# Kernel optimization log

Measured on AMD Instinct MI355X. Metric: run time of the kernel, lower is better.

The kernel has to match this reference:

```python
import jax, jax.numpy as jnp
import numpy as np

BS, SEQ, DK = 4, 4096, 128

def setup_inputs() -> dict:
    key = jax.random.key(0)
    kq, kk, kv = jax.random.split(key, 3)
    q = jax.random.normal(kq, (BS, SEQ, DK), dtype=jnp.float32)
    k = jax.random.normal(kk, (BS, SEQ, DK), dtype=jnp.float32)
    v = jax.random.normal(kv, (BS, SEQ, DK), dtype=jnp.float32)
    return {"q": q, "k": k, "v": v}

def reference(q, k, v):
    d_k = q.shape[-1]
    # scores: [bs, s_q, s_k]
    scaled = jnp.einsum('bqd,bkd->bqk', q, k) / jnp.sqrt(jnp.asarray(d_k, q.dtype))
    # NOTE: original torch code applies softmax over dim=1 (query axis), faithfully reproduced here.
    attn = jax.nn.softmax(scaled, axis=1)
    return jnp.einsum('bqk,bkd->bqd', attn, v)
```

## Files before the change

kernel.cpp:

```cpp
#include <hip/hip_runtime.h>
#include <hip/hip_bf16.h>

#define BS  4
#define SEQ 4096
#define DK  128

#define C1_SCALE (1.4426950408889634f / 11.313708498984761f)

typedef __attribute__((ext_vector_type(8))) short bf16x8;
typedef __attribute__((ext_vector_type(4))) float f32x4;
typedef unsigned short ushort_t;

__device__ inline unsigned pk_bf16(float a, float b) {
    __hip_bfloat162 h = __float22bfloat162_rn(make_float2(a, b));
    union { __hip_bfloat162 h2; unsigned u; } cv;
    cv.h2 = h;
    return cv.u;
}

__device__ inline bf16x8 pk8(float4 a, float4 b) {
    union { bf16x8 v; unsigned u[4]; } r;
    r.u[0] = pk_bf16(a.x, a.y);
    r.u[1] = pk_bf16(a.z, a.w);
    r.u[2] = pk_bf16(b.x, b.y);
    r.u[3] = pk_bf16(b.z, b.w);
    return r.v;
}

__device__ inline void gld_lds16(const ushort_t* g, ushort_t* l) {
    __builtin_amdgcn_global_load_lds(
        (const __attribute__((address_space(1))) unsigned int*)g,
        (__attribute__((address_space(3))) unsigned int*)l,
        16, 0, 0);
}

__device__ inline void bar_fence() {
    __builtin_amdgcn_s_barrier();
    asm volatile("" ::: "memory");
}

__global__ __launch_bounds__(256) void cast_qk_sw(
    const float* __restrict__ Q, const float* __restrict__ K,
    ushort_t* __restrict__ Qb, ushort_t* __restrict__ Kb)
{
    const int g = blockIdx.x * 256 + threadIdx.x;
    const int q = g >> 4, ap = g & 15;
    const int a = ap ^ (q & 15);
    const float* src = Q + (size_t)q * DK + a * 8;
    float4 x = *(const float4*)src, y = *(const float4*)(src + 4);
    x.x *= C1_SCALE; x.y *= C1_SCALE; x.z *= C1_SCALE; x.w *= C1_SCALE;
    y.x *= C1_SCALE; y.y *= C1_SCALE; y.z *= C1_SCALE; y.w *= C1_SCALE;
    *(bf16x8*)(Qb + (size_t)g * 8) = pk8(x, y);
    src = K + (size_t)q * DK + a * 8;
    float4 x2 = *(const float4*)src, y2 = *(const float4*)(src + 4);
    *(bf16x8*)(Kb + (size_t)g * 8) = pk8(x2, y2);
}

__global__ __launch_bounds__(256) void sdpa_lsum(
    const ushort_t* __restrict__ Qb, const ushort_t* __restrict__ Kb,
    float* __restrict__ lp)
{
    __shared__ ushort_t Qs[3][4096];

    const int kt = blockIdx.x, qs = blockIdx.y, b = blockIdx.z;
    const int tid = threadIdx.x;
    const int w = tid >> 6, lane = tid & 63, ln = lane & 15, quad = lane >> 4;

    bf16x8 ka[2][4];
#pragma unroll
    for (int mt = 0; mt < 2; ++mt)
#pragma unroll
        for (int c = 0; c < 4; ++c)
            ka[mt][c] = *(const bf16x8*)(Kb +
                ((size_t)(b * SEQ) + kt * 128 + w * 32 + mt * 16 + ln) * DK +
                (((c * 4 + quad) ^ ln) * 8));

    float ls[2][4] = {};
    const ushort_t* qtb = Qb + ((size_t)(b * SEQ + qs * 512)) * DK;

#define A_DMA(BUF, I)                                                          \
    {                                                                          \
        _Pragma("unroll")                                                      \
        for (int j = 0; j < 2; ++j)                                            \
            gld_lds16(qtb + (size_t)(I) * 4096 + (j * 256 + tid) * 8,          \
                      &Qs[BUF][(j * 256 + w * 64) * 8]);                       \
    }

#define A_CMP(BUF)                                                             \
    {                                                                          \
        bf16x8 qf[2][4];                                                       \
        _Pragma("unroll")                                                      \
        for (int nt = 0; nt < 2; ++nt)                                         \
            _Pragma("unroll")                                                  \
            for (int c = 0; c < 4; ++c)                                        \
                qf[nt][c] = *(const bf16x8*)&Qs[BUF][(nt * 16 + ln) * 128 +    \
                                    (((c * 4 + quad) ^ ln) * 8)];              \
        _Pragma("unroll")                                                      \
        for (int mt = 0; mt < 2; ++mt)                                         \
            _Pragma("unroll")                                                  \
            for (int nt = 0; nt < 2; ++nt) {                                   \
                f32x4 s = {0.f, 0.f, 0.f, 0.f};                                \
                __builtin_amdgcn_s_setprio(1);                                 \
                _Pragma("unroll")                                              \
                for (int c = 0; c < 4; ++c)                                    \
                    s = __builtin_amdgcn_mfma_f32_16x16x32_bf16(               \
                        ka[mt][c], qf[nt][c], s, 0, 0, 0);                     \
                __builtin_amdgcn_s_setprio(0);                                 \
                _Pragma("unroll")                                              \
                for (int r = 0; r < 4; ++r)                                    \
                    ls[mt][r] += __builtin_amdgcn_exp2f(s[r]);                 \
            }                                                                  \
    }

    A_DMA(0, 0)
    A_DMA(1, 1)
    for (int t = 0; t < 15; ++t) {
        asm volatile("s_waitcnt vmcnt(2) lgkmcnt(0)" ::: "memory");
        bar_fence();
        if (t < 14) A_DMA((t + 2) % 3, t + 2)
        A_CMP(t % 3)
    }
    asm volatile("s_waitcnt vmcnt(0) lgkmcnt(0)" ::: "memory");
    bar_fence();
    A_CMP(0)
#undef A_DMA
#undef A_CMP

#pragma unroll
    for (int mt = 0; mt < 2; ++mt)
#pragma unroll
        for (int r = 0; r < 4; ++r) {
            float vv = ls[mt][r];
            vv += __shfl_xor(vv, 1);
            vv += __shfl_xor(vv, 2);
            vv += __shfl_xor(vv, 4);
            vv += __shfl_xor(vv, 8);
            ls[mt][r] = vv;
        }
    if (ln < 8) {
        int k = kt * 128 + w * 32 + (ln >> 2) * 16 + quad * 4 + (ln & 3);
        lp[((size_t)(qs * BS + b)) * SEQ + k] = ls[ln >> 2][ln & 3];
    }
}

__global__ __launch_bounds__(256) void vb_transpose(
    const float* __restrict__ V, const float* __restrict__ lp,
    ushort_t* __restrict__ VbT)
{
    __shared__ float Vl[64][132];
    __shared__ float Wl[64];

    const int kt = blockIdx.x, b = blockIdx.y;
    const int tid = threadIdx.x;
    const int k0 = kt * 64;
    {
        int r = tid >> 2, sg = tid & 3;
        const float* src = V + ((size_t)(b * SEQ) + k0 + r) * DK + sg * 32;
#pragma unroll
        for (int i = 0; i < 8; ++i)
            *(float4*)&Vl[r][sg * 32 + i * 4] = *(const float4*)(src + i * 4);
    }
    if (tid < 64) {
        float s = 0.f;
#pragma unroll
        for (int qs = 0; qs < 8; ++qs)
            s += lp[((size_t)(qs * BS + b)) * SEQ + k0 + tid];
        Wl[tid] = 1.0f / s;
    }
    __syncthreads();

    const int d = tid >> 1, kh = tid & 1;
    unsigned u[16];
#pragma unroll
    for (int j = 0; j < 16; ++j) {
        int row = kh * 32 + j * 2;
        u[j] = pk_bf16(Vl[row][d] * Wl[row], Vl[row + 1][d] * Wl[row + 1]);
    }
    ushort_t* dst = VbT + ((size_t)(b * DK) + d) * SEQ + k0 + kh * 32;
#pragma unroll
    for (int i = 0; i < 4; ++i) {
        uint4 t4; t4.x = u[i*4]; t4.y = u[i*4+1]; t4.z = u[i*4+2]; t4.w = u[i*4+3];
        *(uint4*)(dst + i * 8) = t4;
    }
}

__global__ __launch_bounds__(256) void sdpa_out(
    const ushort_t* __restrict__ Qb, const ushort_t* __restrict__ Kb,
    const ushort_t* __restrict__ VbT,
    float* __restrict__ Op, float* __restrict__ O, int use_partial)
{
    __shared__ ushort_t Kt[2][8192];
    __shared__ ushort_t Vt[2][8192];
    __shared__ ushort_t Pt[4096];

    const int g  = blockIdx.x;
    const int qt = blockIdx.y;
    const int ks = g >> 2, b = g & 3;
    const int tid = threadIdx.x;
    const int w = tid >> 6, lane = tid & 63, ln = lane & 15, quad = lane >> 4;

    bf16x8 qa[4][4];
#pragma unroll
    for (int nt = 0; nt < 4; ++nt)
#pragma unroll
        for (int c = 0; c < 4; ++c)
            qa[c][nt] = *(const bf16x8*)(Qb +
                ((size_t)(b * SEQ) + qt * 64 + nt * 16 + ln) * DK +
                (((c * 4 + quad) ^ ln) * 8));

    f32x4 acc[4][2];
#pragma unroll
    for (int i = 0; i < 4; ++i)
#pragma unroll
        for (int j = 0; j < 2; ++j) acc[i][j] = (f32x4){0.f, 0.f, 0.f, 0.f};

    const ushort_t* ksrc = Kb + ((size_t)(b * SEQ) + ks * 1024) * DK;
    const ushort_t* vsrc = VbT + ((size_t)(b * DK)) * SEQ + ks * 1024;
    const int vd = tid >> 3, vap = tid & 7;

#define O_DMA(BUF, PH)                                                         \
    {                                                                          \
        _Pragma("unroll")                                                      \
        for (int j = 0; j < 4; ++j)                                            \
            gld_lds16(ksrc + (size_t)(PH) * 64 * DK + (j * 256 + tid) * 8,     \
                      &Kt[BUF][(j * 256 + w * 64) * 8]);                       \
        _Pragma("unroll")                                                      \
        for (int j = 0; j < 4; ++j)                                            \
            gld_lds16(vsrc + (size_t)(j * 32 + vd) * SEQ + (PH) * 64 +         \
                          ((vap ^ (vd & 7)) * 8),                              \
                      &Vt[BUF][(j * 256 + w * 64) * 8]);                       \
    }

#define QK_PHASE(BUF)                                                          \
    {                                                                          \
        bf16x8 kf[4];                                                          \
        _Pragma("unroll")                                                      \
        for (int c = 0; c < 4; ++c)                                            \
            kf[c] = *(const bf16x8*)&Kt[BUF][(w * 16 + ln) * 128 +             \
                                             (((c * 4 + quad) ^ ln) * 8)];     \
        _Pragma("unroll")                                                      \
        for (int nt = 0; nt < 4; ++nt) {                                       \
            f32x4 s = {0.f, 0.f, 0.f, 0.f};                                    \
            __builtin_amdgcn_s_setprio(1);                                     \
            _Pragma("unroll")                                                  \
            for (int c = 0; c < 4; ++c)                                        \
                s = __builtin_amdgcn_mfma_f32_16x16x32_bf16(kf[c], qa[c][nt], s, 0, 0, 0); \
            __builtin_amdgcn_s_setprio(0);                                     \
            uint2 pw;                                                          \
            pw.x = pk_bf16(__builtin_amdgcn_exp2f(s[0]),                       \
                           __builtin_amdgcn_exp2f(s[1]));                      \
            pw.y = pk_bf16(__builtin_amdgcn_exp2f(s[2]),                       \
                           __builtin_amdgcn_exp2f(s[3]));                      \
            const int q = nt * 16 + ln;                                        \
            const int a16 = w * 2 + (quad >> 1);                               \
            *(uint2*)&Pt[q * 64 + ((a16 ^ (q & 7)) * 8) + (quad & 1) * 4] = pw; \
        }                                                                      \
    }

#define PV_PHASE(BUF)                                                          \
    {                                                                          \
        _Pragma("unroll")                                                      \
        for (int kc = 0; kc < 2; ++kc) {                                       \
            bf16x8 pa[4], vfr[2];                                              \
            _Pragma("unroll")                                                  \
            for (int qf2 = 0; qf2 < 4; ++qf2)                                  \
                pa[qf2] = *(const bf16x8*)&Pt[(qf2 * 16 + ln) * 64 +           \
                                    (((kc * 4 + quad) ^ (ln & 7)) * 8)];       \
            _Pragma("unroll")                                                  \
            for (int dt = 0; dt < 2; ++dt)                                     \
                vfr[dt] = *(const bf16x8*)&Vt[BUF][(w * 32 + dt * 16 + ln) * 64 + \
                                    (((kc * 4 + quad) ^ (ln & 7)) * 8)];       \
            __builtin_amdgcn_s_setprio(1);                                     \
            _Pragma("unroll")                                                  \
            for (int qf2 = 0; qf2 < 4; ++qf2)                                  \
                _Pragma("unroll")                                              \
                for (int dt = 0; dt < 2; ++dt)                                 \
                    acc[qf2][dt] = __builtin_amdgcn_mfma_f32_16x16x32_bf16(    \
                        pa[qf2], vfr[dt], acc[qf2][dt], 0, 0, 0);              \
            __builtin_amdgcn_s_setprio(0);                                     \
        }                                                                      \
    }

    O_DMA(0, 0)
    O_DMA(1, 1)
    for (int ph = 0; ph < 15; ++ph) {
        const int cur = ph & 1;
        asm volatile("s_waitcnt vmcnt(8)" ::: "memory");
        bar_fence();
        QK_PHASE(cur)
        asm volatile("s_waitcnt lgkmcnt(0)" ::: "memory");
        bar_fence();
        PV_PHASE(cur)
        asm volatile("s_waitcnt lgkmcnt(0)" ::: "memory");
        bar_fence();
        if (ph < 14) O_DMA(cur, ph + 2)
    }
    asm volatile("s_waitcnt vmcnt(0)" ::: "memory");
    bar_fence();
    QK_PHASE(1)
    asm volatile("s_waitcnt lgkmcnt(0)" ::: "memory");
    bar_fence();
    PV_PHASE(1)
#undef O_DMA
#undef QK_PHASE
#undef PV_PHASE

    if (use_partial) {
        float* dst = Op + (size_t)ks * ((size_t)BS * SEQ * DK) +
                     ((size_t)(b * SEQ) + qt * 64 + quad * 4) * DK + w * 32 + ln;
#pragma unroll
        for (int qf2 = 0; qf2 < 4; ++qf2)
#pragma unroll
            for (int dt = 0; dt < 2; ++dt)
#pragma unroll
                for (int r = 0; r < 4; ++r)
                    dst[((size_t)(qf2 * 16 + r)) * DK + dt * 16] = acc[qf2][dt][r];
    } else {
#pragma unroll
        for (int qf2 = 0; qf2 < 4; ++qf2)
#pragma unroll
            for (int dt = 0; dt < 2; ++dt)
#pragma unroll
                for (int r = 0; r < 4; ++r)
                    atomicAdd(&O[((size_t)(b * SEQ) + qt * 64 + qf2 * 16 + quad * 4 + r) * DK +
                                 w * 32 + dt * 16 + ln], acc[qf2][dt][r]);
    }
}

__global__ __launch_bounds__(256) void reduce4(
    const float* __restrict__ Op, float* __restrict__ O)
{
    const size_t N = (size_t)BS * SEQ * DK;
    size_t i = ((size_t)blockIdx.x * 256 + threadIdx.x) * 4;
    float4 a0 = *(const float4*)(Op + i);
    float4 a1 = *(const float4*)(Op + N + i);
    float4 a2 = *(const float4*)(Op + 2 * N + i);
    float4 a3 = *(const float4*)(Op + 3 * N + i);
    float4 r;
    r.x = a0.x + a1.x + a2.x + a3.x;
    r.y = a0.y + a1.y + a2.y + a3.y;
    r.z = a0.z + a1.z + a2.z + a3.z;
    r.w = a0.w + a1.w + a2.w + a3.w;
    *(float4*)(O + i) = r;
}

extern "C" void kernel_launch(void* const* d_in, const int* in_sizes, int n_in,
                              void* d_out, int out_size, void* d_ws, size_t ws_size,
                              hipStream_t stream) {
    const float* q = (const float*)d_in[0];
    const float* k = (const float*)d_in[1];
    const float* v = (const float*)d_in[2];
    float* out = (float*)d_out;

    const size_t QKV = (size_t)BS * SEQ * DK;
    float*    lp  = (float*)d_ws;
    ushort_t* Qb  = (ushort_t*)((char*)d_ws + (1 << 20));
    ushort_t* Kb  = Qb + QKV;
    ushort_t* VbT = Kb + QKV;
    float*    Op  = (float*)(VbT + QKV);

    const size_t need_p = (1u << 20) + 3 * QKV * 2 + 4 * QKV * sizeof(float);

    cast_qk_sw<<<dim3(BS * SEQ * 16 / 256), 256, 0, stream>>>(q, k, Qb, Kb);
    sdpa_lsum  <<<dim3(32, 8, 4), 256, 0, stream>>>(Qb, Kb, lp);
    vb_transpose<<<dim3(64, 4),   256, 0, stream>>>(v, lp, VbT);

    if (ws_size >= need_p) {
        sdpa_out<<<dim3(16, 64), 256, 0, stream>>>(Qb, Kb, VbT, Op, out, 1);
        reduce4 <<<dim3(BS * SEQ * DK / 4 / 256), 256, 0, stream>>>(Op, out);
    } else {
        hipMemsetAsync(out, 0, QKV * sizeof(float), stream);
        sdpa_out<<<dim3(16, 64), 256, 0, stream>>>(Qb, Kb, VbT, nullptr, out, 0);
    }
}
```

Baseline: 153.1 us.

## Software-pipeline QK and PV phases in sdpa_out and halve key splits

Restructures the sdpa_out main loop so the QK scores and exponentials for the next tile are computed while PV runs on the current tile. P is double-buffered in LDS and the exp results are held in registers across iterations, which cuts the barriers per tile from three to one. Key splitting drops from 4 to 2 chunks of 2048 keys, halving the partial-output buffer and reduce traffic but also halving the grid to 512 blocks. Launch bounds now request 2 blocks per CU, which adds register pressure and LDS use in exchange for overlap.

```diff
diff --git a/kernel.cpp b/kernel.cpp
--- a/kernel.cpp
+++ b/kernel.cpp
@@ -184,20 +184,21 @@
     }
 }
 
-__global__ __launch_bounds__(256) void sdpa_out(
+__global__ __launch_bounds__(256, 2) void sdpa_out(
     const ushort_t* __restrict__ Qb, const ushort_t* __restrict__ Kb,
     const ushort_t* __restrict__ VbT,
     float* __restrict__ Op, float* __restrict__ O, int use_partial)
 {
     __shared__ ushort_t Kt[2][8192];
     __shared__ ushort_t Vt[2][8192];
-    __shared__ ushort_t Pt[4096];
+    __shared__ ushort_t Pt[2][4096];
 
     const int g  = blockIdx.x;
     const int qt = blockIdx.y;
     const int ks = g >> 2, b = g & 3;
     const int tid = threadIdx.x;
     const int w = tid >> 6, lane = tid & 63, ln = lane & 15, quad = lane >> 4;
+    const int vd2 = lane >> 3, va2 = lane & 7;
 
     bf16x8 qa[4][4];
 #pragma unroll
@@ -214,24 +215,27 @@
 #pragma unroll
         for (int j = 0; j < 2; ++j) acc[i][j] = (f32x4){0.f, 0.f, 0.f, 0.f};
 
-    const ushort_t* ksrc = Kb + ((size_t)(b * SEQ) + ks * 1024) * DK;
-    const ushort_t* vsrc = VbT + ((size_t)(b * DK)) * SEQ + ks * 1024;
-    const int vd = tid >> 3, vap = tid & 7;
-
-#define O_DMA(BUF, PH)                                                         \
+    const ushort_t* ksrc = Kb + ((size_t)(b * SEQ) + ks * 2048) * DK;
+    const ushort_t* vsrc = VbT + ((size_t)(b * DK)) * SEQ + ks * 2048;
+
+#define DMA_K(BUF, T)                                                          \
     {                                                                          \
         _Pragma("unroll")                                                      \
         for (int j = 0; j < 4; ++j)                                            \
-            gld_lds16(ksrc + (size_t)(PH) * 64 * DK + (j * 256 + tid) * 8,     \
-                      &Kt[BUF][(j * 256 + w * 64) * 8]);                       \
+            gld_lds16(ksrc + ((size_t)(T) * 64 + w * 16 + j * 4 + quad) * DK + \
+                          ln * 8,                                              \
+                      &Kt[BUF][(w * 256 + j * 64) * 8]);                       \
+    }
+#define DMA_V(BUF, T)                                                          \
+    {                                                                          \
         _Pragma("unroll")                                                      \
         for (int j = 0; j < 4; ++j)                                            \
-            gld_lds16(vsrc + (size_t)(j * 32 + vd) * SEQ + (PH) * 64 +         \
-                          ((vap ^ (vd & 7)) * 8),                              \
-                      &Vt[BUF][(j * 256 + w * 64) * 8]);                       \
-    }
-
-#define QK_PHASE(BUF)                                                          \
+            gld_lds16(vsrc + (size_t)(w * 32 + j * 8 + vd2) * SEQ +            \
+                          (T) * 64 + ((va2 ^ vd2) * 8),                        \
+                      &Vt[BUF][(w * 256 + j * 64) * 8]);                       \
+    }
+
+#define QK_COMPUTE(BUF, PW)                                                    \
     {                                                                          \
         bf16x8 kf[4];                                                          \
         _Pragma("unroll")                                                      \
@@ -246,14 +250,20 @@
             for (int c = 0; c < 4; ++c)                                        \
                 s = __builtin_amdgcn_mfma_f32_16x16x32_bf16(kf[c], qa[c][nt], s, 0, 0, 0); \
             __builtin_amdgcn_s_setprio(0);                                     \
-            uint2 pw;                                                          \
-            pw.x = pk_bf16(__builtin_amdgcn_exp2f(s[0]),                       \
-                           __builtin_amdgcn_exp2f(s[1]));                      \
-            pw.y = pk_bf16(__builtin_amdgcn_exp2f(s[2]),                       \
-                           __builtin_amdgcn_exp2f(s[3]));                      \
+            PW[nt].x = pk_bf16(__builtin_amdgcn_exp2f(s[0]),                   \
+                               __builtin_amdgcn_exp2f(s[1]));                  \
+            PW[nt].y = pk_bf16(__builtin_amdgcn_exp2f(s[2]),                   \
+                               __builtin_amdgcn_exp2f(s[3]));                  \
+        }                                                                      \
+    }
+
+#define PT_WRITE(PW, P)                                                        \
+    {                                                                          \
+        _Pragma("unroll")                                                      \
+        for (int nt = 0; nt < 4; ++nt) {                                       \
             const int q = nt * 16 + ln;                                        \
             const int a16 = w * 2 + (quad >> 1);                               \
-            *(uint2*)&Pt[q * 64 + ((a16 ^ (q & 7)) * 8) + (quad & 1) * 4] = pw; \
+            *(uint2*)&Pt[P][q * 64 + ((a16 ^ (q & 7)) * 8) + (quad & 1) * 4] = PW[nt]; \
         }                                                                      \
     }
 
@@ -264,7 +274,7 @@
             bf16x8 pa[4], vfr[2];                                              \
             _Pragma("unroll")                                                  \
             for (int qf2 = 0; qf2 < 4; ++qf2)                                  \
-                pa[qf2] = *(const bf16x8*)&Pt[(qf2 * 16 + ln) * 64 +           \
+                pa[qf2] = *(const bf16x8*)&Pt[BUF][(qf2 * 16 + ln) * 64 +      \
                                     (((kc * 4 + quad) ^ (ln & 7)) * 8)];       \
             _Pragma("unroll")                                                  \
             for (int dt = 0; dt < 2; ++dt)                                     \
@@ -281,28 +291,46 @@
         }                                                                      \
     }
 
-    O_DMA(0, 0)
-    O_DMA(1, 1)
-    for (int ph = 0; ph < 15; ++ph) {
-        const int cur = ph & 1;
-        asm volatile("s_waitcnt vmcnt(8)" ::: "memory");
-        bar_fence();
-        QK_PHASE(cur)
-        asm volatile("s_waitcnt lgkmcnt(0)" ::: "memory");
-        bar_fence();
-        PV_PHASE(cur)
-        asm volatile("s_waitcnt lgkmcnt(0)" ::: "memory");
-        bar_fence();
-        if (ph < 14) O_DMA(cur, ph + 2)
-    }
-    asm volatile("s_waitcnt vmcnt(0)" ::: "memory");
+#define O_ITER(T, CUR, PWRD, PWWR)                                             \
+    {                                                                          \
+        PT_WRITE(PWRD, CUR)                                                    \
+        DMA_K(CUR, (T) + 2)                                                    \
+        asm volatile("s_waitcnt vmcnt(8) lgkmcnt(0)" ::: "memory");            \
+        bar_fence();                                                           \
+        QK_COMPUTE((CUR) ^ 1, PWWR)                                            \
+        PV_PHASE(CUR)                                                          \
+        asm volatile("s_waitcnt lgkmcnt(0)" ::: "memory");                     \
+        DMA_V(CUR, (T) + 2)                                                    \
+    }
+
+    uint2 pwA[4], pwB[4];
+
+    DMA_K(0, 0)
+    DMA_V(0, 0)
+    DMA_K(1, 1)
+    DMA_V(1, 1)
+    asm volatile("s_waitcnt vmcnt(12)" ::: "memory");
+    QK_COMPUTE(0, pwA)
+
+    for (int tt = 0; tt < 15; ++tt) {
+        const int t0 = 2 * tt;
+        O_ITER(t0,     0, pwA, pwB)
+        O_ITER(t0 + 1, 1, pwB, pwA)
+    }
+    PT_WRITE(pwA, 0)
+    asm volatile("s_waitcnt vmcnt(4) lgkmcnt(0)" ::: "memory");
     bar_fence();
-    QK_PHASE(1)
-    asm volatile("s_waitcnt lgkmcnt(0)" ::: "memory");
+    QK_COMPUTE(1, pwB)
+    PV_PHASE(0)
+    PT_WRITE(pwB, 1)
+    asm volatile("s_waitcnt vmcnt(0) lgkmcnt(0)" ::: "memory");
     bar_fence();
     PV_PHASE(1)
-#undef O_DMA
-#undef QK_PHASE
+#undef O_ITER
+#undef DMA_K
+#undef DMA_V
+#undef QK_COMPUTE
+#undef PT_WRITE
 #undef PV_PHASE
 
     if (use_partial) {
@@ -327,20 +355,18 @@
     }
 }
 
-__global__ __launch_bounds__(256) void reduce4(
+__global__ __launch_bounds__(256) void reduce2(
     const float* __restrict__ Op, float* __restrict__ O)
 {
     const size_t N = (size_t)BS * SEQ * DK;
     size_t i = ((size_t)blockIdx.x * 256 + threadIdx.x) * 4;
     float4 a0 = *(const float4*)(Op + i);
     float4 a1 = *(const float4*)(Op + N + i);
-    float4 a2 = *(const float4*)(Op + 2 * N + i);
-    float4 a3 = *(const float4*)(Op + 3 * N + i);
     float4 r;
-    r.x = a0.x + a1.x + a2.x + a3.x;
-    r.y = a0.y + a1.y + a2.y + a3.y;
-    r.z = a0.z + a1.z + a2.z + a3.z;
-    r.w = a0.w + a1.w + a2.w + a3.w;
+    r.x = a0.x + a1.x;
+    r.y = a0.y + a1.y;
+    r.z = a0.z + a1.z;
+    r.w = a0.w + a1.w;
     *(float4*)(O + i) = r;
 }
 
@@ -359,17 +385,17 @@
     ushort_t* VbT = Kb + QKV;
     float*    Op  = (float*)(VbT + QKV);
 
-    const size_t need_p = (1u << 20) + 3 * QKV * 2 + 4 * QKV * sizeof(float);
+    const size_t need_p = (1u << 20) + 3 * QKV * 2 + 2 * QKV * sizeof(float);
 
     cast_qk_sw<<<dim3(BS * SEQ * 16 / 256), 256, 0, stream>>>(q, k, Qb, Kb);
     sdpa_lsum  <<<dim3(32, 8, 4), 256, 0, stream>>>(Qb, Kb, lp);
     vb_transpose<<<dim3(64, 4),   256, 0, stream>>>(v, lp, VbT);
 
     if (ws_size >= need_p) {
-        sdpa_out<<<dim3(16, 64), 256, 0, stream>>>(Qb, Kb, VbT, Op, out, 1);
-        reduce4 <<<dim3(BS * SEQ * DK / 4 / 256), 256, 0, stream>>>(Op, out);
+        sdpa_out<<<dim3(8, 64), 256, 0, stream>>>(Qb, Kb, VbT, Op, out, 1);
+        reduce2<<<dim3(BS * SEQ * DK / 4 / 256), 256, 0, stream>>>(Op, out);
     } else {
         hipMemsetAsync(out, 0, QKV * sizeof(float), stream);
-        sdpa_out<<<dim3(16, 64), 256, 0, stream>>>(Qb, Kb, VbT, nullptr, out, 0);
-    }
-}
+        sdpa_out<<<dim3(8, 64), 256, 0, stream>>>(Qb, Kb, VbT, nullptr, out, 0);
+    }
+}
```

Result: faster. 147.7 us (-3.5%).

## Rewrite sdpa_out with 32x32 MFMA, register-resident P and 128-query tiles

Applied to the files above, without the earlier changes.

The output kernel moves from 16x16x32 to 32x32x16 bf16 MFMA. Each wave now owns 32 query rows, so the block tile grows to 128 queries and the grid is halved. The exponentiated score tile stays in registers and is reshuffled with v_permlane32_swap into the A-operand layout for the PV MFMA, which removes the P round-trip through LDS and one barrier per phase. This cuts LDS traffic and synchronisation and doubles K/V reuse per block. In exchange it raises register pressure (launch_bounds 256,2) and leaves fewer blocks to fill the GPU.

```diff
diff --git a/kernel.cpp b/kernel.cpp
--- a/kernel.cpp
+++ b/kernel.cpp
@@ -9,6 +9,7 @@
 
 typedef __attribute__((ext_vector_type(8))) short bf16x8;
 typedef __attribute__((ext_vector_type(4))) float f32x4;
+typedef __attribute__((ext_vector_type(16))) float f32x16;
 typedef unsigned short ushort_t;
 
 __device__ inline unsigned pk_bf16(float a, float b) {
@@ -37,6 +38,10 @@
 __device__ inline void bar_fence() {
     __builtin_amdgcn_s_barrier();
     asm volatile("" ::: "memory");
+}
+
+__device__ inline void pl32_swap(unsigned &x, unsigned &y) {
+    asm volatile("v_permlane32_swap_b32 %0, %1" : "+v"(x), "+v"(y));
 }
 
 __global__ __launch_bounds__(256) void cast_qk_sw(
@@ -184,146 +189,136 @@
     }
 }
 
-__global__ __launch_bounds__(256) void sdpa_out(
+__global__ __launch_bounds__(256, 2) void sdpa_out(
     const ushort_t* __restrict__ Qb, const ushort_t* __restrict__ Kb,
     const ushort_t* __restrict__ VbT,
     float* __restrict__ Op, float* __restrict__ O, int use_partial)
 {
-    __shared__ ushort_t Kt[2][8192];
-    __shared__ ushort_t Vt[2][8192];
-    __shared__ ushort_t Pt[4096];
+    __shared__ ushort_t Kt[2][64 * 128];
+    __shared__ ushort_t Vt[2][128 * 64];
 
     const int g  = blockIdx.x;
     const int qt = blockIdx.y;
     const int ks = g >> 2, b = g & 3;
     const int tid = threadIdx.x;
-    const int w = tid >> 6, lane = tid & 63, ln = lane & 15, quad = lane >> 4;
-
-    bf16x8 qa[4][4];
-#pragma unroll
-    for (int nt = 0; nt < 4; ++nt)
-#pragma unroll
-        for (int c = 0; c < 4; ++c)
-            qa[c][nt] = *(const bf16x8*)(Qb +
-                ((size_t)(b * SEQ) + qt * 64 + nt * 16 + ln) * DK +
-                (((c * 4 + quad) ^ ln) * 8));
-
-    f32x4 acc[4][2];
+    const int w = tid >> 6, lane = tid & 63;
+    const int l31 = lane & 31, hi = lane >> 5;
+    const int vdn = tid >> 3, van = tid & 7;
+
+    const int qrow = qt * 128 + w * 32 + l31;
+    const ushort_t* qb = Qb + ((size_t)(b * SEQ) + qrow) * DK;
+    bf16x8 qa[8];
+#pragma unroll
+    for (int m = 0; m < 8; ++m)
+        qa[m] = *(const bf16x8*)(qb + (((2 * m + hi) ^ (qrow & 15)) * 8));
+
+    f32x16 acc[4];
 #pragma unroll
     for (int i = 0; i < 4; ++i)
 #pragma unroll
-        for (int j = 0; j < 2; ++j) acc[i][j] = (f32x4){0.f, 0.f, 0.f, 0.f};
+        for (int r = 0; r < 16; ++r) acc[i][r] = 0.f;
 
     const ushort_t* ksrc = Kb + ((size_t)(b * SEQ) + ks * 1024) * DK;
     const ushort_t* vsrc = VbT + ((size_t)(b * DK)) * SEQ + ks * 1024;
-    const int vd = tid >> 3, vap = tid & 7;
-
-#define O_DMA(BUF, PH)                                                         \
+
+#define DMA_KV(BUF, T)                                                         \
     {                                                                          \
         _Pragma("unroll")                                                      \
         for (int j = 0; j < 4; ++j)                                            \
-            gld_lds16(ksrc + (size_t)(PH) * 64 * DK + (j * 256 + tid) * 8,     \
+            gld_lds16(ksrc + (size_t)(T) * 64 * DK + (j * 256 + tid) * 8,      \
                       &Kt[BUF][(j * 256 + w * 64) * 8]);                       \
         _Pragma("unroll")                                                      \
         for (int j = 0; j < 4; ++j)                                            \
-            gld_lds16(vsrc + (size_t)(j * 32 + vd) * SEQ + (PH) * 64 +         \
-                          ((vap ^ (vd & 7)) * 8),                              \
+            gld_lds16(vsrc + (size_t)(j * 32 + vdn) * SEQ + (T) * 64 +         \
+                          ((van ^ (vdn & 7)) * 8),                             \
                       &Vt[BUF][(j * 256 + w * 64) * 8]);                       \
     }
 
-#define QK_PHASE(BUF)                                                          \
+#define SUBTILE(BUF, S)                                                        \
     {                                                                          \
-        bf16x8 kf[4];                                                          \
-        _Pragma("unroll")                                                      \
-        for (int c = 0; c < 4; ++c)                                            \
-            kf[c] = *(const bf16x8*)&Kt[BUF][(w * 16 + ln) * 128 +             \
-                                             (((c * 4 + quad) ^ ln) * 8)];     \
-        _Pragma("unroll")                                                      \
-        for (int nt = 0; nt < 4; ++nt) {                                       \
-            f32x4 s = {0.f, 0.f, 0.f, 0.f};                                    \
+        bf16x8 kf[8];                                                          \
+        _Pragma("unroll")                                                      \
+        for (int m = 0; m < 8; ++m)                                            \
+            kf[m] = *(const bf16x8*)&Kt[BUF][((S) * 32 + l31) * 128 +          \
+                        (((2 * m + hi) ^ (l31 & 15)) * 8)];                    \
+        f32x16 pA, pB;                                                         \
+        _Pragma("unroll")                                                      \
+        for (int r = 0; r < 16; ++r) { pA[r] = 0.f; pB[r] = 0.f; }             \
+        __builtin_amdgcn_s_setprio(1);                                         \
+        _Pragma("unroll")                                                      \
+        for (int m = 0; m < 4; ++m)                                            \
+            pA = __builtin_amdgcn_mfma_f32_32x32x16_bf16(kf[m], qa[m], pA, 0, 0, 0); \
+        _Pragma("unroll")                                                      \
+        for (int m = 0; m < 4; ++m)                                            \
+            pB = __builtin_amdgcn_mfma_f32_32x32x16_bf16(kf[m + 4], qa[m + 4], pB, 0, 0, 0); \
+        __builtin_amdgcn_s_setprio(0);                                         \
+        unsigned wv[8];                                                        \
+        _Pragma("unroll")                                                      \
+        for (int j = 0; j < 8; ++j) {                                          \
+            float e0 = __builtin_amdgcn_exp2f(pA[2 * j]     + pB[2 * j]);      \
+            float e1 = __builtin_amdgcn_exp2f(pA[2 * j + 1] + pB[2 * j + 1]);  \
+            wv[j] = pk_bf16(e0, e1);                                           \
+        }                                                                      \
+        pl32_swap(wv[0], wv[2]); pl32_swap(wv[1], wv[3]);                      \
+        pl32_swap(wv[4], wv[6]); pl32_swap(wv[5], wv[7]);                      \
+        bf16x8 pa0, pa1;                                                       \
+        { union { unsigned u[4]; bf16x8 v; } c;                                \
+          c.u[0] = wv[0]; c.u[1] = wv[1]; c.u[2] = wv[2]; c.u[3] = wv[3];      \
+          pa0 = c.v;                                                           \
+          c.u[0] = wv[4]; c.u[1] = wv[5]; c.u[2] = wv[6]; c.u[3] = wv[7];      \
+          pa1 = c.v; }                                                         \
+        _Pragma("unroll")                                                      \
+        for (int dt = 0; dt < 4; ++dt) {                                       \
+            bf16x8 v0 = *(const bf16x8*)&Vt[BUF][(dt * 32 + l31) * 64 +        \
+                            ((((S) * 4 + 0 + hi) ^ (l31 & 7)) * 8)];           \
+            bf16x8 v1 = *(const bf16x8*)&Vt[BUF][(dt * 32 + l31) * 64 +        \
+                            ((((S) * 4 + 2 + hi) ^ (l31 & 7)) * 8)];           \
             __builtin_amdgcn_s_setprio(1);                                     \
-            _Pragma("unroll")                                                  \
-            for (int c = 0; c < 4; ++c)                                        \
-                s = __builtin_amdgcn_mfma_f32_16x16x32_bf16(kf[c], qa[c][nt], s, 0, 0, 0); \
-            __builtin_amdgcn_s_setprio(0);                                     \
-            uint2 pw;                                                          \
-            pw.x = pk_bf16(__builtin_amdgcn_exp2f(s[0]),                       \
-                           __builtin_amdgcn_exp2f(s[1]));                      \
-            pw.y = pk_bf16(__builtin_amdgcn_exp2f(s[2]),                       \
-                           __builtin_amdgcn_exp2f(s[3]));                      \
-            const int q = nt * 16 + ln;                                        \
-            const int a16 = w * 2 + (quad >> 1);                               \
-            *(uint2*)&Pt[q * 64 + ((a16 ^ (q & 7)) * 8) + (quad & 1) * 4] = pw; \
-        }                                                                      \
-    }
-
-#define PV_PHASE(BUF)                                                          \
-    {                                                                          \
-        _Pragma("unroll")                                                      \
-        for (int kc = 0; kc < 2; ++kc) {                                       \
-            bf16x8 pa[4], vfr[2];                                              \
-            _Pragma("unroll")                                                  \
-            for (int qf2 = 0; qf2 < 4; ++qf2)                                  \
-                pa[qf2] = *(const bf16x8*)&Pt[(qf2 * 16 + ln) * 64 +           \
-                                    (((kc * 4 + quad) ^ (ln & 7)) * 8)];       \
-            _Pragma("unroll")                                                  \
-            for (int dt = 0; dt < 2; ++dt)                                     \
-                vfr[dt] = *(const bf16x8*)&Vt[BUF][(w * 32 + dt * 16 + ln) * 64 + \
-                                    (((kc * 4 + quad) ^ (ln & 7)) * 8)];       \
-            __builtin_amdgcn_s_setprio(1);                                     \
-            _Pragma("unroll")                                                  \
-            for (int qf2 = 0; qf2 < 4; ++qf2)                                  \
-                _Pragma("unroll")                                              \
-                for (int dt = 0; dt < 2; ++dt)                                 \
-                    acc[qf2][dt] = __builtin_amdgcn_mfma_f32_16x16x32_bf16(    \
-                        pa[qf2], vfr[dt], acc[qf2][dt], 0, 0, 0);              \
+            acc[dt] = __builtin_amdgcn_mfma_f32_32x32x16_bf16(v0, pa0, acc[dt], 0, 0, 0); \
+            acc[dt] = __builtin_amdgcn_mfma_f32_32x32x16_bf16(v1, pa1, acc[dt], 0, 0, 0); \
             __builtin_amdgcn_s_setprio(0);                                     \
         }                                                                      \
     }
 
-    O_DMA(0, 0)
-    O_DMA(1, 1)
-    for (int ph = 0; ph < 15; ++ph) {
-        const int cur = ph & 1;
-        asm volatile("s_waitcnt vmcnt(8)" ::: "memory");
+    DMA_KV(0, 0)
+    DMA_KV(1, 1)
+
+    for (int t = 0; t < 16; ++t) {
+        if (t < 15) asm volatile("s_waitcnt vmcnt(8)" ::: "memory");
+        else        asm volatile("s_waitcnt vmcnt(0)" ::: "memory");
         bar_fence();
-        QK_PHASE(cur)
-        asm volatile("s_waitcnt lgkmcnt(0)" ::: "memory");
+        SUBTILE(t & 1, 0)
+        SUBTILE(t & 1, 1)
         bar_fence();
-        PV_PHASE(cur)
-        asm volatile("s_waitcnt lgkmcnt(0)" ::: "memory");
-        bar_fence();
-        if (ph < 14) O_DMA(cur, ph + 2)
-    }
-    asm volatile("s_waitcnt vmcnt(0)" ::: "memory");
-    bar_fence();
-    QK_PHASE(1)
-    asm volatile("s_waitcnt lgkmcnt(0)" ::: "memory");
-    bar_fence();
-    PV_PHASE(1)
-#undef O_DMA
-#undef QK_PHASE
-#undef PV_PHASE
+        if (t < 14) DMA_KV(t & 1, t + 2)
+    }
+#undef DMA_KV
+#undef SUBTILE
 
     if (use_partial) {
         float* dst = Op + (size_t)ks * ((size_t)BS * SEQ * DK) +
-                     ((size_t)(b * SEQ) + qt * 64 + quad * 4) * DK + w * 32 + ln;
-#pragma unroll
-        for (int qf2 = 0; qf2 < 4; ++qf2)
-#pragma unroll
-            for (int dt = 0; dt < 2; ++dt)
-#pragma unroll
-                for (int r = 0; r < 4; ++r)
-                    dst[((size_t)(qf2 * 16 + r)) * DK + dt * 16] = acc[qf2][dt][r];
+                     ((size_t)(b * SEQ) + qrow) * DK;
+#pragma unroll
+        for (int dt = 0; dt < 4; ++dt)
+#pragma unroll
+            for (int gg = 0; gg < 4; ++gg) {
+                float4 v4;
+                v4.x = acc[dt][gg * 4 + 0];
+                v4.y = acc[dt][gg * 4 + 1];
+                v4.z = acc[dt][gg * 4 + 2];
+                v4.w = acc[dt][gg * 4 + 3];
+                *(float4*)(dst + dt * 32 + gg * 8 + hi * 4) = v4;
+            }
     } else {
-#pragma unroll
-        for (int qf2 = 0; qf2 < 4; ++qf2)
-#pragma unroll
-            for (int dt = 0; dt < 2; ++dt)
-#pragma unroll
-                for (int r = 0; r < 4; ++r)
-                    atomicAdd(&O[((size_t)(b * SEQ) + qt * 64 + qf2 * 16 + quad * 4 + r) * DK +
-                                 w * 32 + dt * 16 + ln], acc[qf2][dt][r]);
+        float* dst = O + ((size_t)(b * SEQ) + qrow) * DK;
+#pragma unroll
+        for (int dt = 0; dt < 4; ++dt)
+#pragma unroll
+            for (int gg = 0; gg < 4; ++gg)
+#pragma unroll
+                for (int i = 0; i < 4; ++i)
+                    atomicAdd(dst + dt * 32 + gg * 8 + hi * 4 + i,
+                              acc[dt][gg * 4 + i]);
     }
 }
 
@@ -366,10 +361,10 @@
     vb_transpose<<<dim3(64, 4),   256, 0, stream>>>(v, lp, VbT);
 
     if (ws_size >= need_p) {
-        sdpa_out<<<dim3(16, 64), 256, 0, stream>>>(Qb, Kb, VbT, Op, out, 1);
-        reduce4 <<<dim3(BS * SEQ * DK / 4 / 256), 256, 0, stream>>>(Op, out);
+        sdpa_out<<<dim3(16, 32), 256, 0, stream>>>(Qb, Kb, VbT, Op, out, 1);
+        reduce4<<<dim3(BS * SEQ * DK / 4 / 256), 256, 0, stream>>>(Op, out);
     } else {
         hipMemsetAsync(out, 0, QKV * sizeof(float), stream);
-        sdpa_out<<<dim3(16, 64), 256, 0, stream>>>(Qb, Kb, VbT, nullptr, out, 0);
-    }
-}
+        sdpa_out<<<dim3(16, 32), 256, 0, stream>>>(Qb, Kb, VbT, nullptr, out, 0);
+    }
+}
```

After: 150.1 us. No clear change (-2.0%).

## Materialize exp scores in pass A and replace QK recompute with pure PV pass

Applied to the files above, without the earlier changes.

The first pass now stores the bf16 exponentiated scores to a global workspace while accumulating column sums, so the output kernel no longer recomputes QK^T and exp. The output kernel becomes a triple-buffered streaming P·V GEMM over the full key range per query tile, which removes the split-K partials and the reduce kernel. The cost is writing and re-reading a 128 MB bf16 score matrix through HBM. The grid also shrinks to 256 blocks with 64 serial steps each, and the workspace size check is dropped.

```diff
diff --git a/kernel.cpp b/kernel.cpp
--- a/kernel.cpp
+++ b/kernel.cpp
@@ -56,9 +56,9 @@
     *(bf16x8*)(Kb + (size_t)g * 8) = pk8(x2, y2);
 }
 
-__global__ __launch_bounds__(256) void sdpa_lsum(
+__global__ __launch_bounds__(256) void sdpa_passA(
     const ushort_t* __restrict__ Qb, const ushort_t* __restrict__ Kb,
-    float* __restrict__ lp)
+    ushort_t* __restrict__ Pg, float* __restrict__ lp)
 {
     __shared__ ushort_t Qs[3][4096];
 
@@ -77,6 +77,7 @@
 
     float ls[2][4] = {};
     const ushort_t* qtb = Qb + ((size_t)(b * SEQ + qs * 512)) * DK;
+    ushort_t* pgw = Pg + (((size_t)(b * 64 + qs * 8)) * 64 + kt * 2 + (w >> 1)) * 4096;
 
 #define A_DMA(BUF, I)                                                          \
     {                                                                          \
@@ -86,7 +87,7 @@
                       &Qs[BUF][(j * 256 + w * 64) * 8]);                       \
     }
 
-#define A_CMP(BUF)                                                             \
+#define A_CMP(BUF, T)                                                          \
     {                                                                          \
         bf16x8 qf[2][4];                                                       \
         _Pragma("unroll")                                                      \
@@ -95,6 +96,7 @@
             for (int c = 0; c < 4; ++c)                                        \
                 qf[nt][c] = *(const bf16x8*)&Qs[BUF][(nt * 16 + ln) * 128 +    \
                                     (((c * 4 + quad) ^ ln) * 8)];              \
+        ushort_t* pgt = pgw + (size_t)((T) >> 1) * (64 * 4096);                \
         _Pragma("unroll")                                                      \
         for (int mt = 0; mt < 2; ++mt)                                         \
             _Pragma("unroll")                                                  \
@@ -106,23 +108,30 @@
                     s = __builtin_amdgcn_mfma_f32_16x16x32_bf16(               \
                         ka[mt][c], qf[nt][c], s, 0, 0, 0);                     \
                 __builtin_amdgcn_s_setprio(0);                                 \
-                _Pragma("unroll")                                              \
-                for (int r = 0; r < 4; ++r)                                    \
-                    ls[mt][r] += __builtin_amdgcn_exp2f(s[r]);                 \
+                float e0 = __builtin_amdgcn_exp2f(s[0]);                       \
+                float e1 = __builtin_amdgcn_exp2f(s[1]);                       \
+                float e2 = __builtin_amdgcn_exp2f(s[2]);                       \
+                float e3 = __builtin_amdgcn_exp2f(s[3]);                       \
+                ls[mt][0] += e0; ls[mt][1] += e1;                              \
+                ls[mt][2] += e2; ls[mt][3] += e3;                              \
+                uint2 pw; pw.x = pk_bf16(e0, e1); pw.y = pk_bf16(e2, e3);      \
+                const int ql = (((T) & 1) * 32) + nt * 16 + ln;                \
+                const int aa = (w & 1) * 4 + mt * 2 + (quad >> 1);             \
+                *(uint2*)&pgt[(ql * 8 + (aa ^ (ql & 7))) * 8 + (quad & 1) * 4] = pw; \
             }                                                                  \
     }
 
     A_DMA(0, 0)
     A_DMA(1, 1)
-    for (int t = 0; t < 15; ++t) {
-        asm volatile("s_waitcnt vmcnt(2) lgkmcnt(0)" ::: "memory");
+    for (int t = 0; t < 16; ++t) {
+        if (t == 0)      asm volatile("s_waitcnt vmcnt(2)"  ::: "memory");
+        else if (t == 1) asm volatile("s_waitcnt vmcnt(6)"  ::: "memory");
+        else if (t < 15) asm volatile("s_waitcnt vmcnt(10)" ::: "memory");
+        else             asm volatile("s_waitcnt vmcnt(8)"  ::: "memory");
         bar_fence();
         if (t < 14) A_DMA((t + 2) % 3, t + 2)
-        A_CMP(t % 3)
-    }
-    asm volatile("s_waitcnt vmcnt(0) lgkmcnt(0)" ::: "memory");
-    bar_fence();
-    A_CMP(0)
+        A_CMP(t % 3, t)
+    }
 #undef A_DMA
 #undef A_CMP
 
@@ -184,29 +193,17 @@
     }
 }
 
-__global__ __launch_bounds__(256) void sdpa_out(
-    const ushort_t* __restrict__ Qb, const ushort_t* __restrict__ Kb,
-    const ushort_t* __restrict__ VbT,
-    float* __restrict__ Op, float* __restrict__ O, int use_partial)
-{
-    __shared__ ushort_t Kt[2][8192];
-    __shared__ ushort_t Vt[2][8192];
-    __shared__ ushort_t Pt[4096];
-
-    const int g  = blockIdx.x;
-    const int qt = blockIdx.y;
-    const int ks = g >> 2, b = g & 3;
+__global__ __launch_bounds__(256) void sdpa_pv(
+    const ushort_t* __restrict__ Pg, const ushort_t* __restrict__ VbT,
+    float* __restrict__ O)
+{
+    __shared__ ushort_t Pt[3][4096];
+    __shared__ ushort_t Vt[3][8192];
+
+    const int qt = blockIdx.x, b = blockIdx.y;
     const int tid = threadIdx.x;
     const int w = tid >> 6, lane = tid & 63, ln = lane & 15, quad = lane >> 4;
-
-    bf16x8 qa[4][4];
-#pragma unroll
-    for (int nt = 0; nt < 4; ++nt)
-#pragma unroll
-        for (int c = 0; c < 4; ++c)
-            qa[c][nt] = *(const bf16x8*)(Qb +
-                ((size_t)(b * SEQ) + qt * 64 + nt * 16 + ln) * DK +
-                (((c * 4 + quad) ^ ln) * 8));
+    const int vd = tid >> 3, vap = tid & 7;
 
     f32x4 acc[4][2];
 #pragma unroll
@@ -214,57 +211,30 @@
 #pragma unroll
         for (int j = 0; j < 2; ++j) acc[i][j] = (f32x4){0.f, 0.f, 0.f, 0.f};
 
-    const ushort_t* ksrc = Kb + ((size_t)(b * SEQ) + ks * 1024) * DK;
-    const ushort_t* vsrc = VbT + ((size_t)(b * DK)) * SEQ + ks * 1024;
-    const int vd = tid >> 3, vap = tid & 7;
-
-#define O_DMA(BUF, PH)                                                         \
-    {                                                                          \
+    const ushort_t* psrc = Pg + ((size_t)(b * 64 + qt)) * 64 * 4096;
+    const ushort_t* vsrc = VbT + ((size_t)(b * DK)) * SEQ;
+
+#define B_DMA(BUF, T)                                                          \
+    {                                                                          \
+        _Pragma("unroll")                                                      \
+        for (int j = 0; j < 2; ++j)                                            \
+            gld_lds16(psrc + (size_t)(T) * 4096 + (j * 256 + tid) * 8,         \
+                      &Pt[BUF][(j * 256 + w * 64) * 8]);                       \
         _Pragma("unroll")                                                      \
         for (int j = 0; j < 4; ++j)                                            \
-            gld_lds16(ksrc + (size_t)(PH) * 64 * DK + (j * 256 + tid) * 8,     \
-                      &Kt[BUF][(j * 256 + w * 64) * 8]);                       \
-        _Pragma("unroll")                                                      \
-        for (int j = 0; j < 4; ++j)                                            \
-            gld_lds16(vsrc + (size_t)(j * 32 + vd) * SEQ + (PH) * 64 +         \
+            gld_lds16(vsrc + (size_t)(j * 32 + vd) * SEQ + (T) * 64 +          \
                           ((vap ^ (vd & 7)) * 8),                              \
                       &Vt[BUF][(j * 256 + w * 64) * 8]);                       \
     }
 
-#define QK_PHASE(BUF)                                                          \
-    {                                                                          \
-        bf16x8 kf[4];                                                          \
-        _Pragma("unroll")                                                      \
-        for (int c = 0; c < 4; ++c)                                            \
-            kf[c] = *(const bf16x8*)&Kt[BUF][(w * 16 + ln) * 128 +             \
-                                             (((c * 4 + quad) ^ ln) * 8)];     \
-        _Pragma("unroll")                                                      \
-        for (int nt = 0; nt < 4; ++nt) {                                       \
-            f32x4 s = {0.f, 0.f, 0.f, 0.f};                                    \
-            __builtin_amdgcn_s_setprio(1);                                     \
-            _Pragma("unroll")                                                  \
-            for (int c = 0; c < 4; ++c)                                        \
-                s = __builtin_amdgcn_mfma_f32_16x16x32_bf16(kf[c], qa[c][nt], s, 0, 0, 0); \
-            __builtin_amdgcn_s_setprio(0);                                     \
-            uint2 pw;                                                          \
-            pw.x = pk_bf16(__builtin_amdgcn_exp2f(s[0]),                       \
-                           __builtin_amdgcn_exp2f(s[1]));                      \
-            pw.y = pk_bf16(__builtin_amdgcn_exp2f(s[2]),                       \
-                           __builtin_amdgcn_exp2f(s[3]));                      \
-            const int q = nt * 16 + ln;                                        \
-            const int a16 = w * 2 + (quad >> 1);                               \
-            *(uint2*)&Pt[q * 64 + ((a16 ^ (q & 7)) * 8) + (quad & 1) * 4] = pw; \
-        }                                                                      \
-    }
-
-#define PV_PHASE(BUF)                                                          \
+#define B_CMP(BUF)                                                             \
     {                                                                          \
         _Pragma("unroll")                                                      \
         for (int kc = 0; kc < 2; ++kc) {                                       \
             bf16x8 pa[4], vfr[2];                                              \
             _Pragma("unroll")                                                  \
             for (int qf2 = 0; qf2 < 4; ++qf2)                                  \
-                pa[qf2] = *(const bf16x8*)&Pt[(qf2 * 16 + ln) * 64 +           \
+                pa[qf2] = *(const bf16x8*)&Pt[BUF][(qf2 * 16 + ln) * 64 +      \
                                     (((kc * 4 + quad) ^ (ln & 7)) * 8)];       \
             _Pragma("unroll")                                                  \
             for (int dt = 0; dt < 2; ++dt)                                     \
@@ -281,67 +251,26 @@
         }                                                                      \
     }
 
-    O_DMA(0, 0)
-    O_DMA(1, 1)
-    for (int ph = 0; ph < 15; ++ph) {
-        const int cur = ph & 1;
-        asm volatile("s_waitcnt vmcnt(8)" ::: "memory");
+    B_DMA(0, 0)
+    B_DMA(1, 1)
+    for (int t = 0; t < 64; ++t) {
+        if (t < 63) asm volatile("s_waitcnt vmcnt(6)" ::: "memory");
+        else        asm volatile("s_waitcnt vmcnt(0)" ::: "memory");
         bar_fence();
-        QK_PHASE(cur)
-        asm volatile("s_waitcnt lgkmcnt(0)" ::: "memory");
-        bar_fence();
-        PV_PHASE(cur)
-        asm volatile("s_waitcnt lgkmcnt(0)" ::: "memory");
-        bar_fence();
-        if (ph < 14) O_DMA(cur, ph + 2)
-    }
-    asm volatile("s_waitcnt vmcnt(0)" ::: "memory");
-    bar_fence();
-    QK_PHASE(1)
-    asm volatile("s_waitcnt lgkmcnt(0)" ::: "memory");
-    bar_fence();
-    PV_PHASE(1)
-#undef O_DMA
-#undef QK_PHASE
-#undef PV_PHASE
-
-    if (use_partial) {
-        float* dst = Op + (size_t)ks * ((size_t)BS * SEQ * DK) +
-                     ((size_t)(b * SEQ) + qt * 64 + quad * 4) * DK + w * 32 + ln;
-#pragma unroll
-        for (int qf2 = 0; qf2 < 4; ++qf2)
-#pragma unroll
-            for (int dt = 0; dt < 2; ++dt)
-#pragma unroll
-                for (int r = 0; r < 4; ++r)
-                    dst[((size_t)(qf2 * 16 + r)) * DK + dt * 16] = acc[qf2][dt][r];
-    } else {
-#pragma unroll
-        for (int qf2 = 0; qf2 < 4; ++qf2)
-#pragma unroll
-            for (int dt = 0; dt < 2; ++dt)
-#pragma unroll
-                for (int r = 0; r < 4; ++r)
-                    atomicAdd(&O[((size_t)(b * SEQ) + qt * 64 + qf2 * 16 + quad * 4 + r) * DK +
-                                 w * 32 + dt * 16 + ln], acc[qf2][dt][r]);
-    }
-}
-
-__global__ __launch_bounds__(256) void reduce4(
-    const float* __restrict__ Op, float* __restrict__ O)
-{
-    const size_t N = (size_t)BS * SEQ * DK;
-    size_t i = ((size_t)blockIdx.x * 256 + threadIdx.x) * 4;
-    float4 a0 = *(const float4*)(Op + i);
-    float4 a1 = *(const float4*)(Op + N + i);
-    float4 a2 = *(const float4*)(Op + 2 * N + i);
-    float4 a3 = *(const float4*)(Op + 3 * N + i);
-    float4 r;
-    r.x = a0.x + a1.x + a2.x + a3.x;
-    r.y = a0.y + a1.y + a2.y + a3.y;
-    r.z = a0.z + a1.z + a2.z + a3.z;
-    r.w = a0.w + a1.w + a2.w + a3.w;
-    *(float4*)(O + i) = r;
+        if (t < 62) B_DMA((t + 2) % 3, t + 2)
+        B_CMP(t % 3)
+    }
+#undef B_DMA
+#undef B_CMP
+
+    float* dst = O + ((size_t)(b * SEQ) + qt * 64 + quad * 4) * DK + w * 32 + ln;
+#pragma unroll
+    for (int qf2 = 0; qf2 < 4; ++qf2)
+#pragma unroll
+        for (int dt = 0; dt < 2; ++dt)
+#pragma unroll
+            for (int r = 0; r < 4; ++r)
+                dst[((size_t)(qf2 * 16 + r)) * DK + dt * 16] = acc[qf2][dt][r];
 }
 
 extern "C" void kernel_launch(void* const* d_in, const int* in_sizes, int n_in,
@@ -357,19 +286,11 @@
     ushort_t* Qb  = (ushort_t*)((char*)d_ws + (1 << 20));
     ushort_t* Kb  = Qb + QKV;
     ushort_t* VbT = Kb + QKV;
-    float*    Op  = (float*)(VbT + QKV);
-
-    const size_t need_p = (1u << 20) + 3 * QKV * 2 + 4 * QKV * sizeof(float);
-
-    cast_qk_sw<<<dim3(BS * SEQ * 16 / 256), 256, 0, stream>>>(q, k, Qb, Kb);
-    sdpa_lsum  <<<dim3(32, 8, 4), 256, 0, stream>>>(Qb, Kb, lp);
+    ushort_t* Pg  = VbT + QKV;
+    (void)ws_size;
+
+    cast_qk_sw <<<dim3(BS * SEQ * 16 / 256), 256, 0, stream>>>(q, k, Qb, Kb);
+    sdpa_passA <<<dim3(32, 8, 4), 256, 0, stream>>>(Qb, Kb, Pg, lp);
     vb_transpose<<<dim3(64, 4),   256, 0, stream>>>(v, lp, VbT);
-
-    if (ws_size >= need_p) {
-        sdpa_out<<<dim3(16, 64), 256, 0, stream>>>(Qb, Kb, VbT, Op, out, 1);
-        reduce4 <<<dim3(BS * SEQ * DK / 4 / 256), 256, 0, stream>>>(Op, out);
-    } else {
-        hipMemsetAsync(out, 0, QKV * sizeof(float), stream);
-        sdpa_out<<<dim3(16, 64), 256, 0, stream>>>(Qb, Kb, VbT, nullptr, out, 0);
-    }
-}
+    sdpa_pv    <<<dim3(64, 4),    256, 0, stream>>>(Pg, VbT, out);
+}
```

After: 166.4 us. +8.7%, slower.
